# Kernel optimization log

Measured on AMD Instinct MI355X. Metric: run time of the kernel, lower is better.

## Reference

```python
import jax, jax.numpy as jnp
import numpy as np

BS, N, T, D, R = 64, 256, 32, 512, 8
DK = D // R  # 64 == key_feature_dim


def setup_inputs() -> dict:
    key = jax.random.key(0)
    ks = jax.random.split(key, 20)
    s = 0.02
    p = lambda k, shape: jax.random.normal(k, shape, jnp.float32) * s
    return {
        "v": jax.random.normal(ks[0], (BS, N, D), jnp.float32),
        "b": jax.random.normal(ks[1], (BS, N, D), jnp.float32),
        "v_mask": jnp.ones((BS, N), jnp.float32),
        "t": jax.random.normal(ks[2], (BS, T, D), jnp.float32),
        "t_mask": jnp.ones((BS, T), jnp.float32),
        "WG1_w": p(ks[3], (D, D)), "WG1_b": p(ks[4], (D,)),
        "WG2_w": p(ks[5], (D, D)), "WG2_b": p(ks[6], (D,)),
        "WK_w": p(ks[7], (D, D)), "WK_b": p(ks[8], (D,)),
        "WQ_w": p(ks[9], (D, D)), "WQ_b": p(ks[10], (D,)),
        "WV_w": p(ks[11], (D, D)), "WV_b": p(ks[12], (D,)),
        "tc_w": p(ks[13], (D, 1)), "tc_b": p(ks[14], (1,)),
        "tmap_w": p(ks[15], (D, N * N)), "tmap_b": p(ks[16], (N * N,)),
    }


def _forward(v, b, v_mask, t, t_mask,
             WG1_w, WG1_b, WG2_w, WG2_b, WK_w, WK_b, WQ_w, WQ_b, WV_w, WV_b,
             tc_w, tc_b, tmap_w, tmap_b):
    bs, num_obj, dim = v.shape
    n_rel = R
    dk = dim // n_rel  # dim_per_rel == dim_k

    def shape4(x):  # (bs, N, D) -> (bs, R, N, dk)
        return x.reshape(bs, num_obj, n_rel, dk).transpose(0, 2, 1, 3)

    # --- text summary branch ---
    t_m = t * t_mask[:, :, None]                       # (bs, T, D)
    tc = t_m @ tc_w + tc_b                             # (bs, T, 1)
    tc = jnp.where(t_mask[:, :, None] == 0, -jnp.inf, tc)
    t_sscore = jax.nn.sigmoid(tc)                      # sigmoid(-inf) = 0 for pad
    t_summary = jnp.einsum('btd,bt->bd', t_m, t_sscore[..., 0])   # (bs, D)
    tmap = jax.nn.relu(t_summary @ tmap_w + tmap_b)
    tmap = tmap.reshape(bs, 1, num_obj, num_obj)       # broadcast over relations

    # --- geometric pairwise score ---
    wg1 = shape4((b @ WG1_w + WG1_b) * v_mask[:, :, None])
    wg2 = shape4((b @ WG2_w + WG2_b) * v_mask[:, :, None])
    w_g = jax.nn.relu(jnp.einsum('brnd,brmd->brnm', wg1, wg2)) + tmap

    # --- scaled dot-product score ---
    wk = shape4(v @ WK_w + WK_b)
    wq = shape4(v @ WQ_w + WQ_b)
    scaled_dot = jnp.einsum('brnd,brmd->brnm', wk, wq) / jnp.sqrt(jnp.float32(dk))

    # --- combine, mask, softmax, weighted sum ---
    w_mn = jnp.log(jnp.maximum(w_g, 1e-6)) + scaled_dot
    w_mn = jnp.where((v_mask == 0)[:, None, None, :], -jnp.inf, w_mn)
    attn = jax.nn.softmax(w_mn, axis=-1)               # (bs, R, N, N)

    wv = shape4(v @ WV_w + WV_b)
    out = jnp.einsum('brnm,brmd->brnd', attn, wv)
    out = out.transpose(0, 2, 1, 3).reshape(bs, num_obj, dim)
    return out + v


def reference(v, b, v_mask, t, t_mask,
              WG1_w, WG1_b, WG2_w, WG2_b, WK_w, WK_b, WQ_w, WQ_b, WV_w, WV_b,
              tc_w, tc_b, tmap_w, tmap_b):
    return _forward(v, b, v_mask, t, t_mask,
                    WG1_w, WG1_b, WG2_w, WG2_b, WK_w, WK_b, WQ_w, WQ_b,
                    WV_w, WV_b, tc_w, tc_b, tmap_w, tmap_b)
```

## Files before the change

kernel.cpp:

```cpp
#include <hip/hip_runtime.h>
#include <math.h>

#define BS 64
#define NOBJ 256
#define TTOK 32
#define DIM 512
#define NREL 8
#define DKK 64
#define NN 65536

typedef __attribute__((ext_vector_type(8))) short bf16x8;
typedef __attribute__((ext_vector_type(4))) float f32x4;

__device__ __forceinline__ unsigned short f2bf(float x) {
    union { float f; unsigned int u; } c; c.f = x;
    unsigned int u = c.u;
    return (unsigned short)((u + 0x7fffu + ((u >> 16) & 1u)) >> 16);
}
__device__ __forceinline__ float bf2f(unsigned short h) {
    union { unsigned int u; float f; } c; c.u = ((unsigned int)h) << 16;
    return c.f;
}
__device__ __forceinline__ void gl2lds16(const unsigned short* g, unsigned short* l) {
    __builtin_amdgcn_global_load_lds((const __attribute__((address_space(1))) void*)g,
                                     (__attribute__((address_space(3))) void*)l, 16, 0, 0);
}

__global__ void k_text(const float* __restrict__ tt, const float* __restrict__ t_mask,
                       const float* __restrict__ tc_w, const float* __restrict__ tc_b,
                       unsigned short* __restrict__ ts_bf) {
    int b = blockIdx.x;
    int tid = threadIdx.x;
    __shared__ float red[TTOK][8];
    __shared__ float sc[TTOK];
    {
        int tok = tid >> 3, seg = tid & 7;
        const float* tp = tt + (size_t)(b * TTOK + tok) * DIM + seg * 64;
        const float* wp = tc_w + seg * 64;
        float s = 0.f;
#pragma unroll
        for (int i = 0; i < 16; ++i) {
            float4 a = *(const float4*)(tp + i * 4);
            float4 w = *(const float4*)(wp + i * 4);
            s += a.x * w.x + a.y * w.y + a.z * w.z + a.w * w.w;
        }
        red[tok][seg] = s;
    }
    __syncthreads();
    if (tid < TTOK) {
        float s = 0.f;
#pragma unroll
        for (int i = 0; i < 8; ++i) s += red[tid][i];
        float m = t_mask[b * TTOK + tid];
        float tc = m * s + tc_b[0];
        float sig = 1.f / (1.f + __expf(-tc));
        sc[tid] = (m != 0.f) ? m * sig : 0.f;
    }
    __syncthreads();
    for (int d = tid; d < DIM; d += 256) {
        float acc = 0.f;
#pragma unroll
        for (int tok = 0; tok < TTOK; ++tok)
            acc += tt[(size_t)(b * TTOK + tok) * DIM + d] * sc[tok];
        ts_bf[b * DIM + d] = f2bf(acc);
    }
}

__global__ void k_convert(const float* __restrict__ v, const float* __restrict__ b,
                          unsigned short* __restrict__ v_bf, unsigned short* __restrict__ b_bf) {
    const float* src = blockIdx.y ? b : v;
    unsigned short* dst = blockIdx.y ? b_bf : v_bf;
    size_t i = ((size_t)blockIdx.x * 256 + threadIdx.x) * 4;
    float4 a = *(const float4*)(src + i);
    ushort4 o;
    o.x = f2bf(a.x); o.y = f2bf(a.y); o.z = f2bf(a.z); o.w = f2bf(a.w);
    *(ushort4*)(dst + i) = o;
}

__global__ void k_wt(const float* __restrict__ w0, const float* __restrict__ w1,
                     const float* __restrict__ w2, const float* __restrict__ w3,
                     const float* __restrict__ w4, unsigned short* __restrict__ WT) {
    int wsel = blockIdx.z;
    const float* W = wsel == 0 ? w0 : wsel == 1 ? w1 : wsel == 2 ? w2 : wsel == 3 ? w3 : w4;
    int k0 = blockIdx.x * 64, d0 = blockIdx.y * 64;
    __shared__ float tile[64][65];
    int tid = threadIdx.x;
#pragma unroll
    for (int p = 0; p < 16; ++p) {
        int lin = p * 256 + tid;
        int kk = lin >> 6, dd = lin & 63;
        tile[kk][dd] = W[(size_t)(k0 + kk) * DIM + d0 + dd];
    }
    __syncthreads();
    unsigned short* outp = WT + (size_t)wsel * DIM * DIM;
#pragma unroll
    for (int p = 0; p < 16; ++p) {
        int lin = p * 256 + tid;
        int dd = lin >> 6, kk = lin & 63;
        outp[(size_t)(d0 + dd) * DIM + k0 + kk] = f2bf(tile[kk][dd]);
    }
}

__launch_bounds__(256)
__global__ void k_tmap(const unsigned short* __restrict__ ts_bf,
                       const float* __restrict__ tmap_w, const float* __restrict__ tmap_b,
                       unsigned short* __restrict__ tmap) {
    int j0 = blockIdx.x * 64;
    int tid = threadIdx.x;
    int w = tid >> 6, lane = tid & 63, q = lane >> 4, li = lane & 15;
    __shared__ __align__(16) unsigned short Bt[2][64][40];
    f32x4 acc[4];
#pragma unroll
    for (int ct = 0; ct < 4; ++ct) acc[ct] = (f32x4){0.f, 0.f, 0.f, 0.f};

    int rp = tid >> 4, c4 = tid & 15;
    const float* gsrc = tmap_w + (size_t)(2 * rp) * NN + j0 + c4 * 4;
    float4 f0 = *(const float4*)(gsrc);
    float4 f1 = *(const float4*)(gsrc + NN);

    for (int ks = 0; ks < 16; ++ks) {
        int cur = ks & 1;
        {
            float lo[4] = {f0.x, f0.y, f0.z, f0.w};
            float hi[4] = {f1.x, f1.y, f1.z, f1.w};
#pragma unroll
            for (int e = 0; e < 4; ++e) {
                int col = c4 * 4 + e;
                int x = (col >> 3) & 3;
                int pos = (2 * rp) ^ (x * 8);
                unsigned int pk = (unsigned int)f2bf(lo[e]) | ((unsigned int)f2bf(hi[e]) << 16);
                *(unsigned int*)(&Bt[cur][col][pos]) = pk;
            }
        }
        if (ks < 15) {
            const float* g = gsrc + (size_t)(ks + 1) * 32 * NN;
            f0 = *(const float4*)(g);
            f1 = *(const float4*)(g + NN);
        }
        __syncthreads();
        int k0 = ks * 32;
        bf16x8 a = *(const bf16x8*)(ts_bf + (size_t)(w * 16 + li) * DIM + k0 + q * 8);
#pragma unroll
        for (int ct = 0; ct < 4; ++ct) {
            int col = ct * 16 + li;
            int x = (col >> 3) & 3;
            bf16x8 bb = *(const bf16x8*)(&Bt[cur][col][(q ^ x) * 8]);
            acc[ct] = __builtin_amdgcn_mfma_f32_16x16x32_bf16(a, bb, acc[ct], 0, 0, 0);
        }
    }
#pragma unroll
    for (int ct = 0; ct < 4; ++ct) {
        int j = j0 + ct * 16 + li;
        float bias = tmap_b[j];
#pragma unroll
        for (int i = 0; i < 4; ++i) {
            int bb = w * 16 + q * 4 + i;
            float val = fmaxf(acc[ct][i] + bias, 0.f);
            tmap[(size_t)bb * NN + j] = f2bf(val);
        }
    }
}

__launch_bounds__(256)
__global__ void k_proj(const unsigned short* __restrict__ v_bf, const unsigned short* __restrict__ b_bf,
                       const unsigned short* __restrict__ WT,
                       const float* __restrict__ bias0, const float* __restrict__ bias1,
                       const float* __restrict__ bias2, const float* __restrict__ bias3,
                       const float* __restrict__ bias4, const float* __restrict__ v_mask,
                       unsigned short* __restrict__ wg1, unsigned short* __restrict__ wg2,
                       unsigned short* __restrict__ wk, unsigned short* __restrict__ wq,
                       unsigned short* __restrict__ wvT) {
    int bx = blockIdx.x;
    int by = blockIdx.y;
    int m0 = bx * 128;
    int wsel = by >> 2;
    const unsigned short* A = (wsel < 2) ? b_bf : v_bf;
    int tid = threadIdx.x;
    int w = tid >> 6, lane = tid & 63, q = lane >> 4, li = lane & 15;
    int rh = w & 1, ch = w >> 1;

    __shared__ __align__(16) unsigned short smem[32768];

    f32x4 acc[4][4];
#pragma unroll
    for (int rt = 0; rt < 4; ++rt)
#pragma unroll
        for (int ct = 0; ct < 4; ++ct) acc[rt][ct] = (f32x4){0.f, 0.f, 0.f, 0.f};

    const unsigned short* WTb = WT + (size_t)by * 128 * DIM;

    int rl = lane >> 3;
    int lseg = (lane & 7) ^ rl;
    const unsigned short* Agp[4];
    const unsigned short* Bgp[4];
    unsigned short* Alp[4];
    unsigned short* Blp[4];
#pragma unroll
    for (int c4 = 0; c4 < 4; ++c4) {
        int c = w * 4 + c4;
        int row = c * 8 + rl;
        Agp[c4] = A + (size_t)(m0 + row) * DIM + lseg * 8;
        Bgp[c4] = WTb + (size_t)row * DIM + lseg * 8;
        Alp[c4] = smem + c * 512;
        Blp[c4] = smem + 8192 + c * 512;
    }

    int arow = (rh * 64 + li) * 64;
    int brow = (ch * 64 + li) * 64;
    int sseg0 = ((q) ^ (li & 7)) * 8;
    int sseg1 = ((4 + q) ^ (li & 7)) * 8;

#pragma unroll
    for (int c4 = 0; c4 < 4; ++c4) {
        gl2lds16(Agp[c4], Alp[c4]);
        gl2lds16(Bgp[c4], Blp[c4]);
    }
    __syncthreads();

    for (int ks = 0; ks < 8; ++ks) {
        int cur = ks & 1;
        if (ks < 7) {
            int k0 = (ks + 1) * 64;
            int noff = (cur ^ 1) * 16384;
#pragma unroll
            for (int c4 = 0; c4 < 4; ++c4) {
                gl2lds16(Agp[c4] + k0, Alp[c4] + noff);
                gl2lds16(Bgp[c4] + k0, Blp[c4] + noff);
            }
        }
        const unsigned short* Asb = smem + cur * 16384;
        const unsigned short* Bsb = Asb + 8192;
#pragma unroll
        for (int j = 0; j < 2; ++j) {
            int sseg = j ? sseg1 : sseg0;
            bf16x8 af[4], bfr[4];
#pragma unroll
            for (int rt = 0; rt < 4; ++rt)
                af[rt] = *(const bf16x8*)(Asb + arow + rt * 1024 + sseg);
#pragma unroll
            for (int ct = 0; ct < 4; ++ct)
                bfr[ct] = *(const bf16x8*)(Bsb + brow + ct * 1024 + sseg);
#pragma unroll
            for (int rt = 0; rt < 4; ++rt)
#pragma unroll
                for (int ct = 0; ct < 4; ++ct)
                    acc[rt][ct] = __builtin_amdgcn_mfma_f32_16x16x32_bf16(af[rt], bfr[ct], acc[rt][ct], 0, 0, 0);
        }
        __syncthreads();
    }

    const float* bias = wsel == 0 ? bias0 : wsel == 1 ? bias1 : wsel == 2 ? bias2 : wsel == 3 ? bias3 : bias4;
    int dblk = (by & 3) * 128;

    unsigned short (*T)[136] = (unsigned short (*)[136])smem;
    if (wsel < 4) {
#pragma unroll
        for (int ct = 0; ct < 4; ++ct) {
            int d = dblk + ch * 64 + ct * 16 + li;
            float bs = bias[d];
#pragma unroll
            for (int rt = 0; rt < 4; ++rt) {
#pragma unroll
                for (int i = 0; i < 4; ++i) {
                    int nl = rh * 64 + rt * 16 + q * 4 + i;
                    float val = acc[rt][ct][i] + bs;
                    if (wsel < 2) val *= v_mask[m0 + nl];
                    T[nl][ch * 64 + ct * 16 + li] = f2bf(val);
                }
            }
        }
        __syncthreads();
        unsigned short* dstb = wsel == 0 ? wg1 : wsel == 1 ? wg2 : wsel == 2 ? wk : wq;
        int dc = lane & 15;
#pragma unroll
        for (int rr = 0; rr < 8; ++rr) {
            int outer = w * 32 + rr * 4 + (lane >> 4);
            *(bf16x8*)(dstb + (size_t)(m0 + outer) * DIM + dblk + dc * 8) =
                *(const bf16x8*)(&T[outer][dc * 8]);
        }
    } else {
#pragma unroll
        for (int ct = 0; ct < 4; ++ct) {
            int dl = ch * 64 + ct * 16 + li;
            float bs = bias[dblk + dl];
#pragma unroll
            for (int rt = 0; rt < 4; ++rt) {
#pragma unroll
                for (int i = 0; i < 4; ++i) {
                    int nl = rh * 64 + rt * 16 + q * 4 + i;
                    T[dl][nl] = f2bf(acc[rt][ct][i] + bs);
                }
            }
        }
        __syncthreads();
        int b = m0 >> 8, nbase = m0 & 255;
        int dc = lane & 15;
#pragma unroll
        for (int rr = 0; rr < 8; ++rr) {
            int outer = w * 32 + rr * 4 + (lane >> 4);
            int d = dblk + outer;
            int r = d >> 6, dk = d & 63;
            *(bf16x8*)(wvT + ((size_t)(b * NREL + r) * DKK + dk) * NOBJ + nbase + dc * 8) =
                *(const bf16x8*)(&T[outer][dc * 8]);
        }
    }
}

__launch_bounds__(256)
__global__ void k_attn(const unsigned short* __restrict__ wg1, const unsigned short* __restrict__ wg2,
                       const unsigned short* __restrict__ wk, const unsigned short* __restrict__ wq,
                       const unsigned short* __restrict__ wvT,
                       const unsigned short* __restrict__ tmap, const float* __restrict__ v_mask,
                       const float* __restrict__ v, float* __restrict__ out) {
    int L = blockIdx.x;
    int x = L & 7, jj = L >> 3;
    int b = x + 8 * (jj >> 4);
    int inner = jj & 15;
    int r = inner >> 1, half = inner & 1;
    int br = b * NREL + r;

    int tid = threadIdx.x;
    int w = tid >> 6, lane = tid & 63, q = lane >> 4, li = lane & 15;
    int n0 = half * 128 + w * 32;

    __shared__ __align__(16) unsigned short P_lds[4][2][32][36];

    bf16x8 ag[2][2], ak[2][2];
    {
        const unsigned short* g1b = wg1 + (size_t)(b * NOBJ + n0 + li) * DIM + r * DKK + q * 8;
        const unsigned short* kb  = wk  + (size_t)(b * NOBJ + n0 + li) * DIM + r * DKK + q * 8;
#pragma unroll
        for (int rt = 0; rt < 2; ++rt)
#pragma unroll
            for (int kt = 0; kt < 2; ++kt) {
                ag[rt][kt] = *(const bf16x8*)(g1b + (size_t)rt * 16 * DIM + kt * 32);
                ak[rt][kt] = *(const bf16x8*)(kb + (size_t)rt * 16 * DIM + kt * 32);
            }
    }

    f32x4 O[2][4];
    float lsum[2][4];
#pragma unroll
    for (int rt = 0; rt < 2; ++rt) {
#pragma unroll
        for (int dt = 0; dt < 4; ++dt) O[rt][dt] = (f32x4){0.f, 0.f, 0.f, 0.f};
#pragma unroll
        for (int i = 0; i < 4; ++i) lsum[rt][i] = 0.f;
    }

    const unsigned short* tb = tmap + ((size_t)b << 16) + (n0 + q * 4) * 256 + li;

    bf16x8 vbp[4];

    auto qk_softmax = [&](int j, int c0, int buf) {
        bf16x8 bg[2][2], bq[2][2];
        {
            const unsigned short* g2b = wg2 + (size_t)(b * NOBJ + c0 + li) * DIM + r * DKK + q * 8;
            const unsigned short* qb  = wq  + (size_t)(b * NOBJ + c0 + li) * DIM + r * DKK + q * 8;
#pragma unroll
            for (int ct = 0; ct < 2; ++ct)
#pragma unroll
                for (int kt = 0; kt < 2; ++kt) {
                    bg[ct][kt] = *(const bf16x8*)(g2b + (size_t)ct * 16 * DIM + kt * 32);
                    bq[ct][kt] = *(const bf16x8*)(qb + (size_t)ct * 16 * DIM + kt * 32);
                }
        }
        float vm0 = v_mask[b * NOBJ + c0 + li];
        float vm1 = v_mask[b * NOBJ + c0 + 16 + li];

#pragma unroll
        for (int rt = 0; rt < 2; ++rt) {
#pragma unroll
            for (int ct = 0; ct < 2; ++ct) {
                f32x4 aG = (f32x4){0.f, 0.f, 0.f, 0.f};
                f32x4 aK = (f32x4){0.f, 0.f, 0.f, 0.f};
#pragma unroll
                for (int kt = 0; kt < 2; ++kt) {
                    aG = __builtin_amdgcn_mfma_f32_16x16x32_bf16(ag[rt][kt], bg[ct][kt], aG, 0, 0, 0);
                    aK = __builtin_amdgcn_mfma_f32_16x16x32_bf16(ak[rt][kt], bq[ct][kt], aK, 0, 0, 0);
                }
                float vm = ct ? vm1 : vm0;
#pragma unroll
                for (int i = 0; i < 4; ++i) {
                    float tm = bf2f(tb[(rt * 16 + i) * 256 + c0 + ct * 16]);
                    float g = fmaxf(fmaxf(aG[i], 0.f) + tm, 1e-6f);
                    float p = (vm == 0.f) ? 0.f : g * __expf(aK[i] * 0.125f);
                    lsum[rt][i] += p;
                    P_lds[w][buf][rt * 16 + q * 4 + i][ct * 16 + li] = f2bf(p);
                }
            }
        }
    };
    auto load_vb = [&](int c0) {
#pragma unroll
        for (int dt = 0; dt < 4; ++dt)
            vbp[dt] = *(const bf16x8*)(wvT + (size_t)(br * DKK + dt * 16 + li) * NOBJ + c0 + q * 8);
    };
    auto pv = [&](int buf) {
        bf16x8 pa[2];
#pragma unroll
        for (int rt = 0; rt < 2; ++rt)
            pa[rt] = *(const bf16x8*)(&P_lds[w][buf][rt * 16 + li][q * 8]);
#pragma unroll
        for (int rt = 0; rt < 2; ++rt)
#pragma unroll
            for (int dt = 0; dt < 4; ++dt)
                O[rt][dt] = __builtin_amdgcn_mfma_f32_16x16x32_bf16(pa[rt], vbp[dt], O[rt][dt], 0, 0, 0);
    };

    qk_softmax(0, 0, 0);
    load_vb(0);

    for (int j = 1; j < 8; ++j) {
        int c0 = j * 32;
        pv((j - 1) & 1);
        qk_softmax(j, c0, j & 1);
        load_vb(c0);
    }
    pv(1);

#pragma unroll
    for (int rt = 0; rt < 2; ++rt) {
        float linv[4];
#pragma unroll
        for (int i = 0; i < 4; ++i) {
            float s = lsum[rt][i];
            s += __shfl_xor(s, 1);
            s += __shfl_xor(s, 2);
            s += __shfl_xor(s, 4);
            s += __shfl_xor(s, 8);
            linv[i] = 1.f / s;
        }
#pragma unroll
        for (int dt = 0; dt < 4; ++dt) {
#pragma unroll
            for (int i = 0; i < 4; ++i) {
                int n = n0 + rt * 16 + q * 4 + i;
                size_t idx = (size_t)(b * NOBJ + n) * DIM + r * DKK + dt * 16 + li;
                out[idx] = O[rt][dt][i] * linv[i] + v[idx];
            }
        }
    }
}

extern "C" void kernel_launch(void* const* d_in, const int* in_sizes, int n_in,
                              void* d_out, int out_size, void* d_ws, size_t ws_size,
                              hipStream_t stream) {
    const float* v      = (const float*)d_in[0];
    const float* b      = (const float*)d_in[1];
    const float* v_mask = (const float*)d_in[2];
    const float* t      = (const float*)d_in[3];
    const float* t_mask = (const float*)d_in[4];
    const float* WG1_w  = (const float*)d_in[5];
    const float* WG1_b  = (const float*)d_in[6];
    const float* WG2_w  = (const float*)d_in[7];
    const float* WG2_b  = (const float*)d_in[8];
    const float* WK_w   = (const float*)d_in[9];
    const float* WK_b   = (const float*)d_in[10];
    const float* WQ_w   = (const float*)d_in[11];
    const float* WQ_b   = (const float*)d_in[12];
    const float* WV_w   = (const float*)d_in[13];
    const float* WV_b   = (const float*)d_in[14];
    const float* tc_w   = (const float*)d_in[15];
    const float* tc_b   = (const float*)d_in[16];
    const float* tmap_w = (const float*)d_in[17];
    const float* tmap_b = (const float*)d_in[18];
    float* out = (float*)d_out;

    char* ws = (char*)d_ws;
    size_t off = 0;
    auto alloc = [&](size_t bytes) {
        void* p = ws + off;
        off += (bytes + 255) & ~(size_t)255;
        return p;
    };
    unsigned short* ts_bf = (unsigned short*)alloc((size_t)BS * DIM * 2);
    unsigned short* tmap  = (unsigned short*)alloc((size_t)BS * NN * 2);
    unsigned short* v_bf  = (unsigned short*)alloc((size_t)BS * NOBJ * DIM * 2);
    unsigned short* b_bf  = (unsigned short*)alloc((size_t)BS * NOBJ * DIM * 2);
    unsigned short* WT    = (unsigned short*)alloc((size_t)5 * DIM * DIM * 2);
    unsigned short* wg1   = (unsigned short*)alloc((size_t)BS * NOBJ * DIM * 2);
    unsigned short* wg2   = (unsigned short*)alloc((size_t)BS * NOBJ * DIM * 2);
    unsigned short* wk    = (unsigned short*)alloc((size_t)BS * NOBJ * DIM * 2);
    unsigned short* wq    = (unsigned short*)alloc((size_t)BS * NOBJ * DIM * 2);
    unsigned short* wvT   = (unsigned short*)alloc((size_t)BS * NOBJ * DIM * 2);

    k_text<<<dim3(BS), dim3(256), 0, stream>>>(t, t_mask, tc_w, tc_b, ts_bf);
    k_convert<<<dim3(8192, 2), dim3(256), 0, stream>>>(v, b, v_bf, b_bf);
    k_wt<<<dim3(8, 8, 5), dim3(256), 0, stream>>>(WG1_w, WG2_w, WK_w, WQ_w, WV_w, WT);
    k_tmap<<<dim3(1024), dim3(256), 0, stream>>>(ts_bf, tmap_w, tmap_b, tmap);
    k_proj<<<dim3(128, 20), dim3(256), 0, stream>>>(v_bf, b_bf, WT,
                                                    WG1_b, WG2_b, WK_b, WQ_b, WV_b, v_mask,
                                                    wg1, wg2, wk, wq, wvT);
    k_attn<<<dim3(1024), dim3(256), 0, stream>>>(wg1, wg2, wk, wq, wvT, tmap, v_mask, v, out);
}
```

Baseline: 428.9 us.

## Merge preprocessing kernels into one launch and prioritize MFMA waves in attention

Folds the text-summary, bf16 conversion and weight-transpose kernels into a single k_pre launch that picks its role from the block index, removing two kernel launches and their gaps. In the attention kernel, s_setprio raises wave priority around the MFMA sequences, and the V-tile load is issued before the QK/softmax step so it overlaps with that compute. The merged kernel uses the larger shared buffer for every block, which may slightly reduce occupancy for the conversion blocks.

```diff
diff --git a/kernel.cpp b/kernel.cpp
--- a/kernel.cpp
+++ b/kernel.cpp
@@ -26,78 +26,83 @@
                                      (__attribute__((address_space(3))) void*)l, 16, 0, 0);
 }
 
-__global__ void k_text(const float* __restrict__ tt, const float* __restrict__ t_mask,
-                       const float* __restrict__ tc_w, const float* __restrict__ tc_b,
-                       unsigned short* __restrict__ ts_bf) {
-    int b = blockIdx.x;
+__global__ void k_pre(const float* __restrict__ v, const float* __restrict__ bsrc,
+                      unsigned short* __restrict__ v_bf, unsigned short* __restrict__ b_bf,
+                      const float* __restrict__ w0, const float* __restrict__ w1,
+                      const float* __restrict__ w2, const float* __restrict__ w3,
+                      const float* __restrict__ w4, unsigned short* __restrict__ WT,
+                      const float* __restrict__ tt, const float* __restrict__ t_mask,
+                      const float* __restrict__ tc_w, const float* __restrict__ tc_b,
+                      unsigned short* __restrict__ ts_bf) {
+    __shared__ __align__(16) float shbuf[64 * 65];
+    int bid = blockIdx.x;
     int tid = threadIdx.x;
-    __shared__ float red[TTOK][8];
-    __shared__ float sc[TTOK];
-    {
-        int tok = tid >> 3, seg = tid & 7;
-        const float* tp = tt + (size_t)(b * TTOK + tok) * DIM + seg * 64;
-        const float* wp = tc_w + seg * 64;
-        float s = 0.f;
-#pragma unroll
-        for (int i = 0; i < 16; ++i) {
-            float4 a = *(const float4*)(tp + i * 4);
-            float4 w = *(const float4*)(wp + i * 4);
-            s += a.x * w.x + a.y * w.y + a.z * w.z + a.w * w.w;
-        }
-        red[tok][seg] = s;
-    }
-    __syncthreads();
-    if (tid < TTOK) {
-        float s = 0.f;
-#pragma unroll
-        for (int i = 0; i < 8; ++i) s += red[tid][i];
-        float m = t_mask[b * TTOK + tid];
-        float tc = m * s + tc_b[0];
-        float sig = 1.f / (1.f + __expf(-tc));
-        sc[tid] = (m != 0.f) ? m * sig : 0.f;
-    }
-    __syncthreads();
-    for (int d = tid; d < DIM; d += 256) {
-        float acc = 0.f;
-#pragma unroll
-        for (int tok = 0; tok < TTOK; ++tok)
-            acc += tt[(size_t)(b * TTOK + tok) * DIM + d] * sc[tok];
-        ts_bf[b * DIM + d] = f2bf(acc);
-    }
-}
-
-__global__ void k_convert(const float* __restrict__ v, const float* __restrict__ b,
-                          unsigned short* __restrict__ v_bf, unsigned short* __restrict__ b_bf) {
-    const float* src = blockIdx.y ? b : v;
-    unsigned short* dst = blockIdx.y ? b_bf : v_bf;
-    size_t i = ((size_t)blockIdx.x * 256 + threadIdx.x) * 4;
-    float4 a = *(const float4*)(src + i);
-    ushort4 o;
-    o.x = f2bf(a.x); o.y = f2bf(a.y); o.z = f2bf(a.z); o.w = f2bf(a.w);
-    *(ushort4*)(dst + i) = o;
-}
-
-__global__ void k_wt(const float* __restrict__ w0, const float* __restrict__ w1,
-                     const float* __restrict__ w2, const float* __restrict__ w3,
-                     const float* __restrict__ w4, unsigned short* __restrict__ WT) {
-    int wsel = blockIdx.z;
-    const float* W = wsel == 0 ? w0 : wsel == 1 ? w1 : wsel == 2 ? w2 : wsel == 3 ? w3 : w4;
-    int k0 = blockIdx.x * 64, d0 = blockIdx.y * 64;
-    __shared__ float tile[64][65];
-    int tid = threadIdx.x;
-#pragma unroll
-    for (int p = 0; p < 16; ++p) {
-        int lin = p * 256 + tid;
-        int kk = lin >> 6, dd = lin & 63;
-        tile[kk][dd] = W[(size_t)(k0 + kk) * DIM + d0 + dd];
-    }
-    __syncthreads();
-    unsigned short* outp = WT + (size_t)wsel * DIM * DIM;
-#pragma unroll
-    for (int p = 0; p < 16; ++p) {
-        int lin = p * 256 + tid;
-        int dd = lin >> 6, kk = lin & 63;
-        outp[(size_t)(d0 + dd) * DIM + k0 + kk] = f2bf(tile[kk][dd]);
+
+    if (bid < 16384) {
+        const float* src = (bid >= 8192) ? bsrc : v;
+        unsigned short* dst = (bid >= 8192) ? b_bf : v_bf;
+        int bx = bid & 8191;
+        size_t i = ((size_t)bx * 256 + tid) * 4;
+        float4 a = *(const float4*)(src + i);
+        ushort4 o;
+        o.x = f2bf(a.x); o.y = f2bf(a.y); o.z = f2bf(a.z); o.w = f2bf(a.w);
+        *(ushort4*)(dst + i) = o;
+    } else if (bid < 16704) {
+        int idx = bid - 16384;
+        int wsel = idx >> 6;
+        int rem = idx & 63;
+        int k0 = (rem & 7) * 64, d0 = (rem >> 3) * 64;
+        const float* W = wsel == 0 ? w0 : wsel == 1 ? w1 : wsel == 2 ? w2 : wsel == 3 ? w3 : w4;
+        float (*tile)[65] = (float (*)[65])shbuf;
+#pragma unroll
+        for (int p = 0; p < 16; ++p) {
+            int lin = p * 256 + tid;
+            int kk = lin >> 6, dd = lin & 63;
+            tile[kk][dd] = W[(size_t)(k0 + kk) * DIM + d0 + dd];
+        }
+        __syncthreads();
+        unsigned short* outp = WT + (size_t)wsel * DIM * DIM;
+#pragma unroll
+        for (int p = 0; p < 16; ++p) {
+            int lin = p * 256 + tid;
+            int dd = lin >> 6, kk = lin & 63;
+            outp[(size_t)(d0 + dd) * DIM + k0 + kk] = f2bf(tile[kk][dd]);
+        }
+    } else {
+        int b = bid - 16704;
+        float (*red)[8] = (float (*)[8])shbuf;
+        float* sc = shbuf + TTOK * 8;
+        {
+            int tok = tid >> 3, seg = tid & 7;
+            const float* tp = tt + (size_t)(b * TTOK + tok) * DIM + seg * 64;
+            const float* wp = tc_w + seg * 64;
+            float s = 0.f;
+#pragma unroll
+            for (int i = 0; i < 16; ++i) {
+                float4 a = *(const float4*)(tp + i * 4);
+                float4 w = *(const float4*)(wp + i * 4);
+                s += a.x * w.x + a.y * w.y + a.z * w.z + a.w * w.w;
+            }
+            red[tok][seg] = s;
+        }
+        __syncthreads();
+        if (tid < TTOK) {
+            float s = 0.f;
+#pragma unroll
+            for (int i = 0; i < 8; ++i) s += red[tid][i];
+            float m = t_mask[b * TTOK + tid];
+            float tc = m * s + tc_b[0];
+            float sig = 1.f / (1.f + __expf(-tc));
+            sc[tid] = (m != 0.f) ? m * sig : 0.f;
+        }
+        __syncthreads();
+        for (int d = tid; d < DIM; d += 256) {
+            float acc = 0.f;
+#pragma unroll
+            for (int tok = 0; tok < TTOK; ++tok)
+                acc += tt[(size_t)(b * TTOK + tok) * DIM + d] * sc[tok];
+            ts_bf[b * DIM + d] = f2bf(acc);
+        }
     }
 }
 
@@ -352,7 +357,7 @@
 
     bf16x8 vbp[4];
 
-    auto qk_softmax = [&](int j, int c0, int buf) {
+    auto qk_softmax = [&](int c0, int buf) {
         bf16x8 bg[2][2], bq[2][2];
         {
             const unsigned short* g2b = wg2 + (size_t)(b * NOBJ + c0 + li) * DIM + r * DKK + q * 8;
@@ -374,11 +379,13 @@
             for (int ct = 0; ct < 2; ++ct) {
                 f32x4 aG = (f32x4){0.f, 0.f, 0.f, 0.f};
                 f32x4 aK = (f32x4){0.f, 0.f, 0.f, 0.f};
+                __builtin_amdgcn_s_setprio(1);
 #pragma unroll
                 for (int kt = 0; kt < 2; ++kt) {
                     aG = __builtin_amdgcn_mfma_f32_16x16x32_bf16(ag[rt][kt], bg[ct][kt], aG, 0, 0, 0);
                     aK = __builtin_amdgcn_mfma_f32_16x16x32_bf16(ak[rt][kt], bq[ct][kt], aK, 0, 0, 0);
                 }
+                __builtin_amdgcn_s_setprio(0);
                 float vm = ct ? vm1 : vm0;
 #pragma unroll
                 for (int i = 0; i < 4; ++i) {
@@ -401,21 +408,23 @@
 #pragma unroll
         for (int rt = 0; rt < 2; ++rt)
             pa[rt] = *(const bf16x8*)(&P_lds[w][buf][rt * 16 + li][q * 8]);
+        __builtin_amdgcn_s_setprio(1);
 #pragma unroll
         for (int rt = 0; rt < 2; ++rt)
 #pragma unroll
             for (int dt = 0; dt < 4; ++dt)
                 O[rt][dt] = __builtin_amdgcn_mfma_f32_16x16x32_bf16(pa[rt], vbp[dt], O[rt][dt], 0, 0, 0);
+        __builtin_amdgcn_s_setprio(0);
     };
 
-    qk_softmax(0, 0, 0);
     load_vb(0);
+    qk_softmax(0, 0);
 
     for (int j = 1; j < 8; ++j) {
         int c0 = j * 32;
         pv((j - 1) & 1);
-        qk_softmax(j, c0, j & 1);
         load_vb(c0);
+        qk_softmax(c0, j & 1);
     }
     pv(1);
 
@@ -485,9 +494,9 @@
     unsigned short* wq    = (unsigned short*)alloc((size_t)BS * NOBJ * DIM * 2);
     unsigned short* wvT   = (unsigned short*)alloc((size_t)BS * NOBJ * DIM * 2);
 
-    k_text<<<dim3(BS), dim3(256), 0, stream>>>(t, t_mask, tc_w, tc_b, ts_bf);
-    k_convert<<<dim3(8192, 2), dim3(256), 0, stream>>>(v, b, v_bf, b_bf);
-    k_wt<<<dim3(8, 8, 5), dim3(256), 0, stream>>>(WG1_w, WG2_w, WK_w, WQ_w, WV_w, WT);
+    k_pre<<<dim3(16768), dim3(256), 0, stream>>>(v, b, v_bf, b_bf,
+                                                 WG1_w, WG2_w, WK_w, WQ_w, WV_w, WT,
+                                                 t, t_mask, tc_w, tc_b, ts_bf);
     k_tmap<<<dim3(1024), dim3(256), 0, stream>>>(ts_bf, tmap_w, tmap_b, tmap);
     k_proj<<<dim3(128, 20), dim3(256), 0, stream>>>(v_bf, b_bf, WT,
                                                     WG1_b, WG2_b, WK_b, WQ_b, WV_b, v_mask,
```

Result: slower. 449.1 us (+4.7%).
